# Performance work log

Hardware: AMD Instinct MI355X
Metric: run time of the kernel (lower is better)

Reference implementation:

```python
import jax, jax.numpy as jnp
import numpy as np

MAP_DIM = 2048
HIDDEN_DIM = 768


def setup_inputs() -> dict:
    key = jax.random.key(0)
    k = jax.random.split(key, 8)
    maps = jax.random.normal(k[0], (8, 14, 14, MAP_DIM), dtype=jnp.float32)
    hiddens = jax.random.normal(k[1], (8, 64, HIDDEN_DIM), dtype=jnp.float32)
    s_map = 1.0 / np.sqrt(MAP_DIM)
    s_hid = 1.0 / np.sqrt(HIDDEN_DIM)
    W_map = jax.random.uniform(k[2], (HIDDEN_DIM, MAP_DIM), jnp.float32, -s_map, s_map)
    b_map = jax.random.uniform(k[3], (HIDDEN_DIM,), jnp.float32, -s_map, s_map)
    W_final = jax.random.uniform(k[4], (HIDDEN_DIM, MAP_DIM), jnp.float32, -s_map, s_map)
    b_final = jax.random.uniform(k[5], (HIDDEN_DIM,), jnp.float32, -s_map, s_map)
    W_rect = jax.random.uniform(k[6], (1, HIDDEN_DIM), jnp.float32, -s_hid, s_hid)
    b_rect = jax.random.uniform(k[7], (1,), jnp.float32, -s_hid, s_hid)
    return {"maps": maps, "hiddens": hiddens, "W_map": W_map, "b_map": b_map,
            "W_final": W_final, "b_final": b_final, "W_rect": W_rect, "b_rect": b_rect}


def reference(maps, hiddens, W_map, b_map, W_final, b_final, W_rect, b_rect):
    B = maps.shape[0]
    # flatten spatial dims: (B, P, M)
    fm = maps.reshape(B, -1, maps.shape[-1])
    # map_linear: (B, P, H)
    mlo = jnp.einsum('bpm,hm->bph', fm, W_map) + b_map
    # additive (Bahdanau-style) score tensor: (B, T, P, H)
    rect = jax.nn.relu(mlo[:, None, :, :] + hiddens[:, :, None, :])
    # rectified_linear H -> 1, squeeze: (B, T, P)
    scores = jnp.einsum('btph,h->btp', rect, W_rect[0]) + b_rect[0]
    # softmax over pixels
    attn = jax.nn.softmax(scores, axis=2)  # (B, T, P)
    # weighted sum of flattened maps: (B, T, M)
    ctx = jnp.einsum('btp,bpm->btm', attn, fm)
    out = jnp.einsum('btm,hm->bth', ctx, W_final) + b_final + hiddens
    return out, attn
```

## Files before the change

### kernel.cpp

```cpp
#include <hip/hip_runtime.h>
#include <stdint.h>

#define NB 8
#define NP 196
#define NM 2048
#define NH 768
#define NT 64
#define PPAD 224
#define NROWS (NB*NP)
#define HC 16
#define HCL 48

typedef __attribute__((ext_vector_type(8))) short short8;
typedef __attribute__((ext_vector_type(4))) float floatx4;
typedef __fp16 h2 __attribute__((ext_vector_type(2)));

__device__ __forceinline__ uint16_t f2b_(float f){
    union{float f; uint32_t i;} v; v.f=f; uint32_t x=v.i;
    return (uint16_t)((x + 0x7fffu + ((x>>16)&1u))>>16);
}
__device__ __forceinline__ uint16_t f2h_(float f){
    union{__fp16 h; uint16_t u;} v; v.h = (__fp16)f; return v.u;
}
__device__ __forceinline__ h2 u2h2(uint32_t u){ union{uint32_t u; h2 h;} v; v.u=u; return v.h; }
__device__ __forceinline__ short8 ldsfrag(const uint16_t* p){
    union{ uint4 u; short8 s; } v; v.u = *(const uint4*)p; return v.s;
}

__global__ __launch_bounds__(256)
void cvt3(const float* __restrict__ s0, uint16_t* __restrict__ d0, int n0,
          const float* __restrict__ s1, uint16_t* __restrict__ d1, int n1,
          const float* __restrict__ s2, uint16_t* __restrict__ d2, int n2)
{
    long i = (long)(blockIdx.x*256 + threadIdx.x)*8;
    const float* s; uint16_t* d; long j;
    if (i < n0)                { s=s0; d=d0; j=i; }
    else if (i < (long)n0+n1)  { s=s1; d=d1; j=i-n0; }
    else                       { s=s2; d=d2; j=i-n0-n1; if (j>=n2) return; }
    float4 a = *(const float4*)(s+j);
    float4 b = *(const float4*)(s+j+4);
    uint4 w;
    w.x = (uint32_t)f2b_(a.x) | ((uint32_t)f2b_(a.y)<<16);
    w.y = (uint32_t)f2b_(a.z) | ((uint32_t)f2b_(a.w)<<16);
    w.z = (uint32_t)f2b_(b.x) | ((uint32_t)f2b_(b.y)<<16);
    w.w = (uint32_t)f2b_(b.z) | ((uint32_t)f2b_(b.w)<<16);
    *(uint4*)(d+j) = w;
}

#define LSTR 72
__global__ __launch_bounds__(256)
void k1_tiled(const uint16_t* __restrict__ A, const uint16_t* __restrict__ Bcat,
              const float* __restrict__ bmap, uint16_t* __restrict__ mloT,
              uint16_t* __restrict__ gt)
{
    __shared__ uint16_t sA[64*LSTR];
    __shared__ uint16_t sB[64*LSTR];
    const int tid  = threadIdx.x;
    const int wv   = tid >> 6, lane = tid & 63;
    const int quad = lane >> 4, lq = lane & 15;
    const int m0 = blockIdx.x*64, n0 = blockIdx.y*64;

    const int r0 = tid >> 3, q0 = tid & 7;
    const int r1 = r0 + 32;
    int gar0 = m0 + r0; if (gar0 >= NROWS) gar0 = NROWS-1;
    int gar1 = m0 + r1; if (gar1 >= NROWS) gar1 = NROWS-1;
    const uint16_t* pa0 = A + (size_t)gar0*NM + q0*8;
    const uint16_t* pa1 = A + (size_t)gar1*NM + q0*8;
    const uint16_t* pb0 = Bcat + (size_t)(n0 + r0)*NM + q0*8;
    const uint16_t* pb1 = Bcat + (size_t)(n0 + r1)*NM + q0*8;
    uint16_t* la0 = &sA[r0*LSTR + q0*8];
    uint16_t* la1 = &sA[r1*LSTR + q0*8];
    uint16_t* lb0 = &sB[r0*LSTR + q0*8];
    uint16_t* lb1 = &sB[r1*LSTR + q0*8];

    const int msub = (wv & 1)*32, nsub = (wv >> 1)*32;

    floatx4 acc[2][2];
    #pragma unroll
    for (int i=0;i<2;++i)
        #pragma unroll
        for (int j=0;j<2;++j) acc[i][j] = (floatx4){0.f,0.f,0.f,0.f};

    uint4 va0 = *(const uint4*)pa0, va1 = *(const uint4*)pa1;
    uint4 vb0 = *(const uint4*)pb0, vb1 = *(const uint4*)pb1;

    for (int ks=0; ks<32; ++ks){
        *(uint4*)la0 = va0; *(uint4*)la1 = va1;
        *(uint4*)lb0 = vb0; *(uint4*)lb1 = vb1;
        __syncthreads();
        if (ks < 31){
            const int off = (ks+1)*64;
            va0 = *(const uint4*)(pa0 + off);
            va1 = *(const uint4*)(pa1 + off);
            vb0 = *(const uint4*)(pb0 + off);
            vb1 = *(const uint4*)(pb1 + off);
        }
        #pragma unroll
        for (int kk=0; kk<2; ++kk){
            short8 af[2], bf[2];
            #pragma unroll
            for (int mt=0;mt<2;++mt)
                af[mt] = ldsfrag(&sA[(msub + mt*16 + lq)*LSTR + kk*32 + quad*8]);
            #pragma unroll
            for (int nt=0;nt<2;++nt)
                bf[nt] = ldsfrag(&sB[(nsub + nt*16 + lq)*LSTR + kk*32 + quad*8]);
            #pragma unroll
            for (int mt=0;mt<2;++mt)
                #pragma unroll
                for (int nt=0;nt<2;++nt)
                    acc[mt][nt] = __builtin_amdgcn_mfma_f32_16x16x32_bf16(af[mt], bf[nt], acc[mt][nt], 0,0,0);
        }
        __syncthreads();
    }

    if (n0 < NH){
        #pragma unroll
        for (int nt=0;nt<2;++nt){
            const int col = n0 + nsub + nt*16 + lq;
            const float bv = bmap[col];
            #pragma unroll
            for (int mt=0;mt<2;++mt){
                floatx4 c = acc[mt][nt];
                const int rb = m0 + msub + mt*16 + quad*4;
                #pragma unroll
                for (int r=0;r<4;++r){
                    const int row = rb + r;
                    if (row < NROWS){
                        const int b = row / NP, p = row - b*NP;
                        mloT[((size_t)b*NH + col)*PPAD + p] = f2h_(c[r] + bv);
                    }
                }
            }
        }
    } else {
        #pragma unroll
        for (int nt=0;nt<2;++nt){
            const int h = n0 - NH + nsub + nt*16 + lq;
            #pragma unroll
            for (int mt=0;mt<2;++mt){
                floatx4 c = acc[mt][nt];
                const int rb = m0 + msub + mt*16 + quad*4;
                #pragma unroll
                for (int r=0;r<4;++r){
                    const int row = rb + r;
                    if (row < NROWS){
                        const int b = row / NP, p = row - b*NP;
                        gt[((size_t)b*NH + h)*PPAD + p] = f2b_(c[r]);
                    }
                }
            }
        }
    }
}

__global__ __launch_bounds__(256)
void k2a(const uint16_t* __restrict__ mloT, const float* __restrict__ hid,
         const float* __restrict__ Wrect, float* __restrict__ partial)
{
    const int hcv = blockIdx.x;
    const int tgp = blockIdx.y;
    const int b   = blockIdx.z;
    const int tid = threadIdx.x;
    const int w   = tid >> 6;
    const int L   = tid & 63;
    const int slot = w & 1;
    const int tg   = tgp*2 + (w>>1);
    const int t0   = tg*8;
    const int Lc   = (slot && L > 47) ? 47 : L;
    const int p    = slot*128 + 2*Lc;

    float acc[8][2];
    #pragma unroll
    for (int i=0;i<8;++i){ acc[i][0]=0.f; acc[i][1]=0.f; }

    const uint16_t* mp = mloT + (size_t)b*NH*PPAD + p;
    const float*    hb = hid + ((size_t)b*NT + t0)*NH;
    const int h0 = hcv*HCL;

    #pragma unroll 4
    for (int hh=0; hh<HCL; ++hh){
        const int h = h0 + hh;
        const uint32_t m = *(const uint32_t*)(mp + (size_t)h*PPAD);
        const h2 mh = u2h2(m);
        const float m0f = (float)mh.x;
        const float m1f = (float)mh.y;
        const float wvv = Wrect[h];
        #pragma unroll
        for (int ti=0; ti<8; ++ti){
            const float hv = hb[(size_t)ti*NH + h];
            acc[ti][0] = fmaf(fmaxf(m0f+hv, 0.f), wvv, acc[ti][0]);
            acc[ti][1] = fmaf(fmaxf(m1f+hv, 0.f), wvv, acc[ti][1]);
        }
    }
    #pragma unroll
    for (int ti=0; ti<8; ++ti){
        float2 v = make_float2(acc[ti][0], acc[ti][1]);
        *(float2*)&partial[(((size_t)hcv*NB + b)*NT + t0+ti)*PPAD + p] = v;
    }
}

__global__ __launch_bounds__(256)
void k2b(const float* __restrict__ partial, float* __restrict__ attn_out,
         uint16_t* __restrict__ attnb)
{
    const int bt = blockIdx.x;
    const int tid = threadIdx.x;
    const int lane = tid & 63, wv = tid >> 6;
    __shared__ float s_red[8];

    float s = 0.f;
    if (tid < PPAD){
        #pragma unroll
        for (int hcv=0; hcv<HC; ++hcv)
            s += partial[(((size_t)hcv*NB*NT) + bt)*PPAD + tid];
    }
    float v = (tid < NP) ? s : -3.0e38f;
    #pragma unroll
    for (int off=32; off>0; off>>=1) v = fmaxf(v, __shfl_xor(v, off));
    if (lane == 0) s_red[wv] = v;
    __syncthreads();
    const float mx = fmaxf(fmaxf(s_red[0], s_red[1]), fmaxf(s_red[2], s_red[3]));
    float e = (tid < NP) ? __expf(s - mx) : 0.f;
    float r = e;
    #pragma unroll
    for (int off=32; off>0; off>>=1) r += __shfl_xor(r, off);
    if (lane == 0) s_red[4 + wv] = r;
    __syncthreads();
    const float inv = 1.f / (s_red[4] + s_red[5] + s_red[6] + s_red[7]);
    const float a = e * inv;
    if (tid < NP)   attn_out[(size_t)bt*NP + tid] = a;
    if (tid < PPAD) attnb[(size_t)bt*PPAD + tid] = (tid < NP) ? f2b_(a) : (uint16_t)0;
}

__global__ __launch_bounds__(64)
void k4_small(const uint16_t* __restrict__ attnb, const uint16_t* __restrict__ gt,
              const float* __restrict__ bfin, const float* __restrict__ hid,
              float* __restrict__ out)
{
    const int lane = threadIdx.x;
    const int quad = lane>>4, lq = lane&15;
    const int tt = blockIdx.x;
    const int n0 = blockIdx.y*64;
    const int b  = blockIdx.z;
    const uint16_t* aprow = attnb + ((size_t)b*NT + tt*16 + lq)*PPAD + quad*8;
    const uint16_t* bp[4];
    #pragma unroll
    for (int i=0;i<4;++i) bp[i] = gt + ((size_t)b*NH + n0 + i*16 + lq)*PPAD + quad*8;

    floatx4 acc[4];
    #pragma unroll
    for (int i=0;i<4;++i) acc[i] = (floatx4){0.f,0.f,0.f,0.f};
    #pragma unroll
    for (int ks=0; ks<7; ++ks){
        short8 Af = ldsfrag(aprow + ks*32);
        #pragma unroll
        for (int i=0;i<4;++i)
            acc[i] = __builtin_amdgcn_mfma_f32_16x16x32_bf16(Af, ldsfrag(bp[i] + ks*32), acc[i], 0,0,0);
    }
    #pragma unroll
    for (int ns=0;ns<4;++ns){
        const int col = n0 + ns*16 + lq;
        const float bv = bfin[col];
        floatx4 c = acc[ns];
        #pragma unroll
        for (int r=0;r<4;++r){
            const int row = b*NT + tt*16 + quad*4 + r;
            const size_t idx = (size_t)row*NH + col;
            out[idx] = c[r] + bv + hid[idx];
        }
    }
}

__global__ __launch_bounds__(256)
void k1_map(const float* __restrict__ fm, const float* __restrict__ Wmap,
            const float* __restrict__ bmap, float* __restrict__ mlo)
{
    __shared__ float s_fm[8][NM];
    const int row0 = blockIdx.x*8;
    for (int i=threadIdx.x; i<8*NM; i+=256){
        int r=i>>11, k=i&2047;
        s_fm[r][k] = fm[(size_t)(row0+r)*NM + k];
    }
    __syncthreads();
    #pragma unroll
    for (int it=0; it<3; ++it){
        int c = threadIdx.x + it*256;
        float acc[8];
        #pragma unroll
        for(int r=0;r<8;++r) acc[r]=0.f;
        const float* wr = Wmap + (size_t)c*NM;
        for (int k=0;k<NM;k+=4){
            float4 w4 = *(const float4*)(wr + k);
            #pragma unroll
            for(int r=0;r<8;++r){
                acc[r]=fmaf(w4.x,s_fm[r][k+0],acc[r]);
                acc[r]=fmaf(w4.y,s_fm[r][k+1],acc[r]);
                acc[r]=fmaf(w4.z,s_fm[r][k+2],acc[r]);
                acc[r]=fmaf(w4.w,s_fm[r][k+3],acc[r]);
            }
        }
        float bb = bmap[c];
        for(int r=0;r<8;++r) mlo[(size_t)(row0+r)*NH + c] = acc[r]+bb;
    }
}

__global__ __launch_bounds__(256)
void k2_scores_f(const float* __restrict__ mlo, const float* __restrict__ hid,
                 const float* __restrict__ Wrect, const float* __restrict__ brect,
                 float* __restrict__ attn_out)
{
    const int b    = blockIdx.x >> 4;
    const int tg   = blockIdx.x & 15;
    const int wave = threadIdx.x >> 6;
    const int lane = threadIdx.x & 63;
    const int t    = tg*4 + wave;
    float hv[12], wv[12];
    #pragma unroll
    for (int j=0;j<12;++j){
        int h = lane + 64*j;
        hv[j] = hid[(size_t)(b*NT+t)*NH + h];
        wv[j] = Wrect[h];
    }
    __shared__ float s_sc[4][NP];
    for (int p=0;p<NP;++p){
        const float* mr = mlo + ((size_t)b*NP + p)*NH;
        float acc = 0.f;
        #pragma unroll
        for (int j=0;j<12;++j){
            float v = fmaxf(mr[lane+64*j] + hv[j], 0.f);
            acc = fmaf(v,wv[j],acc);
        }
        #pragma unroll
        for (int off=32; off>0; off>>=1) acc += __shfl_down(acc,off);
        if (lane==0) s_sc[wave][p] = acc;
    }
    __syncthreads();
    float x[4]; int pidx[4];
    #pragma unroll
    for (int i=0;i<4;++i){
        int p = lane + 64*i; pidx[i]=p;
        x[i] = (p<NP) ? s_sc[wave][p] : -3.0e38f;
    }
    float mx = fmaxf(fmaxf(x[0],x[1]),fmaxf(x[2],x[3]));
    #pragma unroll
    for (int off=32; off>0; off>>=1) mx = fmaxf(mx,__shfl_xor(mx,off));
    float sum=0.f;
    #pragma unroll
    for (int i=0;i<4;++i){ x[i] = (pidx[i]<NP) ? __expf(x[i]-mx) : 0.f; sum += x[i]; }
    #pragma unroll
    for (int off=32; off>0; off>>=1) sum += __shfl_xor(sum,off);
    const float inv = 1.f/sum;
    const size_t base = (size_t)(b*NT+t)*NP;
    #pragma unroll
    for (int i=0;i<4;++i) if (pidx[i]<NP) attn_out[base+pidx[i]] = x[i]*inv;
}

__global__ __launch_bounds__(256)
void k3_ctx(const float* __restrict__ attn, const float* __restrict__ fm,
            float* __restrict__ ctx)
{
    const int b  = blockIdx.x >> 4;
    const int tg = blockIdx.x & 15;
    __shared__ float s_a[4][NP];
    for (int i=threadIdx.x; i<4*NP; i+=256){
        int tt=i/NP, p=i-tt*NP;
        s_a[tt][p] = attn[(size_t)(b*NT + tg*4+tt)*NP + p];
    }
    __syncthreads();
    const int m0 = threadIdx.x*8;
    float acc[4][8];
    #pragma unroll
    for(int tt=0;tt<4;++tt)
        #pragma unroll
        for(int i=0;i<8;++i) acc[tt][i]=0.f;
    const float* fb = fm + (size_t)b*NP*NM + m0;
    for (int p=0;p<NP;++p){
        float4 u0 = *(const float4*)(fb + (size_t)p*NM);
        float4 u1 = *(const float4*)(fb + (size_t)p*NM + 4);
        float f[8] = {u0.x,u0.y,u0.z,u0.w,u1.x,u1.y,u1.z,u1.w};
        #pragma unroll
        for(int tt=0;tt<4;++tt){
            float a = s_a[tt][p];
            #pragma unroll
            for(int i=0;i<8;++i) acc[tt][i] = fmaf(a,f[i],acc[tt][i]);
        }
    }
    #pragma unroll
    for(int tt=0;tt<4;++tt){
        float* cr = ctx + (size_t)(b*NT + tg*4+tt)*NM + m0;
        #pragma unroll
        for(int i=0;i<8;++i) cr[i]=acc[tt][i];
    }
}

__global__ __launch_bounds__(256)
void k4_final(const float* __restrict__ ctx, const float* __restrict__ Wfin,
              const float* __restrict__ bfin, const float* __restrict__ hid,
              float* __restrict__ out)
{
    __shared__ float s_c[8][NM];
    const int row0 = blockIdx.x*8;
    for (int i=threadIdx.x; i<8*NM; i+=256){
        int r=i>>11, k=i&2047;
        s_c[r][k] = ctx[(size_t)(row0+r)*NM + k];
    }
    __syncthreads();
    #pragma unroll
    for (int it=0; it<3; ++it){
        int c = threadIdx.x + it*256;
        float acc[8];
        #pragma unroll
        for(int r=0;r<8;++r) acc[r]=0.f;
        const float* wr = Wfin + (size_t)c*NM;
        for (int k=0;k<NM;k+=4){
            float4 w4 = *(const float4*)(wr + k);
            #pragma unroll
            for(int r=0;r<8;++r){
                acc[r]=fmaf(w4.x,s_c[r][k+0],acc[r]);
                acc[r]=fmaf(w4.y,s_c[r][k+1],acc[r]);
                acc[r]=fmaf(w4.z,s_c[r][k+2],acc[r]);
                acc[r]=fmaf(w4.w,s_c[r][k+3],acc[r]);
            }
        }
        float bb = bfin[c];
        for(int r=0;r<8;++r)
            out[(size_t)(row0+r)*NH + c] = acc[r] + bb + hid[(size_t)(row0+r)*NH + c];
    }
}

extern "C" void kernel_launch(void* const* d_in, const int* in_sizes, int n_in,
                              void* d_out, int out_size, void* d_ws, size_t ws_size,
                              hipStream_t stream)
{
    const float* maps  = (const float*)d_in[0];
    const float* hid   = (const float*)d_in[1];
    const float* Wmap  = (const float*)d_in[2];
    const float* bmap  = (const float*)d_in[3];
    const float* Wfin  = (const float*)d_in[4];
    const float* bfin  = (const float*)d_in[5];
    const float* Wrect = (const float*)d_in[6];
    const float* brect = (const float*)d_in[7];

    float* out_ptr  = (float*)d_out;
    float* attn_out = out_ptr + (size_t)NB*NT*NH;

    const int    FME    = NB*NP*NM;
    const int    WE     = NH*NM;
    const size_t fmb_b  = (size_t)FME*2;
    const size_t w_b    = (size_t)WE*2;
    const size_t mloT_b = (size_t)NB*NH*PPAD*2;
    const size_t gt_b   = (size_t)NB*NH*PPAD*2;
    const size_t atb_b  = (size_t)NB*NT*PPAD*2;
    const size_t need   = fmb_b + 2*w_b + mloT_b + gt_b + atb_b;

    if (ws_size >= need) {
        uint16_t* fmb   = (uint16_t*)d_ws;
        uint16_t* wcat  = (uint16_t*)((char*)d_ws + fmb_b);
        uint16_t* wfinb = wcat + (size_t)WE;
        uint16_t* mloT  = (uint16_t*)((char*)d_ws + fmb_b + 2*w_b);
        uint16_t* gt    = mloT + (size_t)NB*NH*PPAD;
        uint16_t* attnb = gt   + (size_t)NB*NH*PPAD;
        float*    partial = (float*)d_ws;

        const int total8 = (FME + 2*WE)/8;
        hipLaunchKernelGGL(cvt3, dim3(total8/256), dim3(256), 0, stream,
                           maps, fmb, FME, Wmap, wcat, WE, Wfin, wfinb, WE);
        hipLaunchKernelGGL(k1_tiled, dim3(25,24), dim3(256), 0, stream,
                           fmb, wcat, bmap, mloT, gt);
        hipLaunchKernelGGL(k2a, dim3(HC,4,NB), dim3(256), 0, stream,
                           mloT, hid, Wrect, partial);
        hipLaunchKernelGGL(k2b, dim3(NB*NT), dim3(256), 0, stream,
                           partial, attn_out, attnb);
        hipLaunchKernelGGL(k4_small, dim3(4,12,NB), dim3(64), 0, stream,
                           attnb, gt, bfin, hid, out_ptr);
    } else {
        float* mlo = (float*)d_ws;
        float* ctx = mlo + (size_t)NB*NP*NH;
        hipLaunchKernelGGL(k1_map,     dim3(NB*NP/8),   dim3(256), 0, stream, maps, Wmap, bmap, mlo);
        hipLaunchKernelGGL(k2_scores_f,dim3(NB*(NT/4)), dim3(256), 0, stream, mlo, hid, Wrect, brect, attn_out);
        hipLaunchKernelGGL(k3_ctx,     dim3(NB*(NT/4)), dim3(256), 0, stream, attn_out, maps, ctx);
        hipLaunchKernelGGL(k4_final,   dim3(NB*NT/8),   dim3(256), 0, stream, ctx, Wfin, bfin, hid, out_ptr);
    }
}
```

Baseline: 136.7 us.

## Use 128x128 GEMM tiles with direct global-to-LDS loads and XOR swizzle

```diff
diff --git a/kernel.cpp b/kernel.cpp
--- a/kernel.cpp
+++ b/kernel.cpp
@@ -25,6 +25,14 @@
 __device__ __forceinline__ h2 u2h2(uint32_t u){ union{uint32_t u; h2 h;} v; v.u=u; return v.h; }
 __device__ __forceinline__ short8 ldsfrag(const uint16_t* p){
     union{ uint4 u; short8 s; } v; v.u = *(const uint4*)p; return v.s;
+}
+__device__ __forceinline__ void gload16(const uint16_t* g, uint16_t* l){
+    __builtin_amdgcn_global_load_lds(
+        reinterpret_cast<const __attribute__((address_space(1))) uint32_t*>(
+            reinterpret_cast<uintptr_t>(g)),
+        reinterpret_cast<__attribute__((address_space(3))) uint32_t*>(
+            reinterpret_cast<uintptr_t>(l)),
+        16, 0, 0);
 }
 
 __global__ __launch_bounds__(256)
@@ -47,106 +55,97 @@
     *(uint4*)(d+j) = w;
 }
 
-#define LSTR 72
-__global__ __launch_bounds__(256)
-void k1_tiled(const uint16_t* __restrict__ A, const uint16_t* __restrict__ Bcat,
-              const float* __restrict__ bmap, uint16_t* __restrict__ mloT,
-              uint16_t* __restrict__ gt)
-{
-    __shared__ uint16_t sA[64*LSTR];
-    __shared__ uint16_t sB[64*LSTR];
-    const int tid  = threadIdx.x;
-    const int wv   = tid >> 6, lane = tid & 63;
-    const int quad = lane >> 4, lq = lane & 15;
-    const int m0 = blockIdx.x*64, n0 = blockIdx.y*64;
-
-    const int r0 = tid >> 3, q0 = tid & 7;
-    const int r1 = r0 + 32;
-    int gar0 = m0 + r0; if (gar0 >= NROWS) gar0 = NROWS-1;
-    int gar1 = m0 + r1; if (gar1 >= NROWS) gar1 = NROWS-1;
-    const uint16_t* pa0 = A + (size_t)gar0*NM + q0*8;
-    const uint16_t* pa1 = A + (size_t)gar1*NM + q0*8;
-    const uint16_t* pb0 = Bcat + (size_t)(n0 + r0)*NM + q0*8;
-    const uint16_t* pb1 = Bcat + (size_t)(n0 + r1)*NM + q0*8;
-    uint16_t* la0 = &sA[r0*LSTR + q0*8];
-    uint16_t* la1 = &sA[r1*LSTR + q0*8];
-    uint16_t* lb0 = &sB[r0*LSTR + q0*8];
-    uint16_t* lb1 = &sB[r1*LSTR + q0*8];
-
-    const int msub = (wv & 1)*32, nsub = (wv >> 1)*32;
-
-    floatx4 acc[2][2];
-    #pragma unroll
-    for (int i=0;i<2;++i)
-        #pragma unroll
-        for (int j=0;j<2;++j) acc[i][j] = (floatx4){0.f,0.f,0.f,0.f};
-
-    uint4 va0 = *(const uint4*)pa0, va1 = *(const uint4*)pa1;
-    uint4 vb0 = *(const uint4*)pb0, vb1 = *(const uint4*)pb1;
+__global__ __launch_bounds__(256)
+void k1_m97(const uint16_t* __restrict__ A, const uint16_t* __restrict__ Bcat,
+            const float* __restrict__ bmap, uint16_t* __restrict__ mloT,
+            uint16_t* __restrict__ gt)
+{
+    __shared__ uint16_t sA[128*64];
+    __shared__ uint16_t sB[128*64];
+    const int tid = threadIdx.x;
+    const int w = tid>>6, lane = tid&63;
+    const int quad = lane>>4, lq = lane&15;
+    const int m0 = blockIdx.x*128, n0 = blockIdx.y*128;
+
+    const int r8 = lane>>3;
+    const int qx = (lane&7) ^ r8;
+    const uint16_t* gsrc[8];
+    uint16_t* ldst[8];
+    #pragma unroll
+    for (int j=0;j<8;++j){
+        const int c = w*8 + j;
+        if (c < 16){
+            gsrc[j] = A + (size_t)(m0 + c*8 + r8)*NM + qx*8;
+            ldst[j] = &sA[c*512];
+        } else {
+            gsrc[j] = Bcat + (size_t)(n0 + (c-16)*8 + r8)*NM + qx*8;
+            ldst[j] = &sB[(c-16)*512];
+        }
+    }
+
+    const int msub = (w&1)*64, nsub = (w>>1)*64;
+    floatx4 acc[16];
+    #pragma unroll
+    for (int i=0;i<16;++i) acc[i] = (floatx4){0.f,0.f,0.f,0.f};
 
     for (int ks=0; ks<32; ++ks){
-        *(uint4*)la0 = va0; *(uint4*)la1 = va1;
-        *(uint4*)lb0 = vb0; *(uint4*)lb1 = vb1;
+        #pragma unroll
+        for (int j=0;j<8;++j) gload16(gsrc[j] + ks*64, ldst[j]);
         __syncthreads();
-        if (ks < 31){
-            const int off = (ks+1)*64;
-            va0 = *(const uint4*)(pa0 + off);
-            va1 = *(const uint4*)(pa1 + off);
-            vb0 = *(const uint4*)(pb0 + off);
-            vb1 = *(const uint4*)(pb1 + off);
-        }
         #pragma unroll
         for (int kk=0; kk<2; ++kk){
-            short8 af[2], bf[2];
-            #pragma unroll
-            for (int mt=0;mt<2;++mt)
-                af[mt] = ldsfrag(&sA[(msub + mt*16 + lq)*LSTR + kk*32 + quad*8]);
-            #pragma unroll
-            for (int nt=0;nt<2;++nt)
-                bf[nt] = ldsfrag(&sB[(nsub + nt*16 + lq)*LSTR + kk*32 + quad*8]);
-            #pragma unroll
-            for (int mt=0;mt<2;++mt)
+            short8 af[4], bf[4];
+            #pragma unroll
+            for (int mt=0;mt<4;++mt){
+                const int r = msub + mt*16 + lq;
+                af[mt] = ldsfrag(&sA[r*64 + (((kk*4+quad) ^ (lq&7))*8)]);
+            }
+            #pragma unroll
+            for (int nt=0;nt<4;++nt){
+                const int r = nsub + nt*16 + lq;
+                bf[nt] = ldsfrag(&sB[r*64 + (((kk*4+quad) ^ (lq&7))*8)]);
+            }
+            #pragma unroll
+            for (int mt=0;mt<4;++mt)
                 #pragma unroll
-                for (int nt=0;nt<2;++nt)
-                    acc[mt][nt] = __builtin_amdgcn_mfma_f32_16x16x32_bf16(af[mt], bf[nt], acc[mt][nt], 0,0,0);
+                for (int nt=0;nt<4;++nt)
+                    acc[mt*4+nt] = __builtin_amdgcn_mfma_f32_16x16x32_bf16(af[mt], bf[nt], acc[mt*4+nt], 0,0,0);
         }
         __syncthreads();
     }
 
     if (n0 < NH){
         #pragma unroll
-        for (int nt=0;nt<2;++nt){
+        for (int nt=0;nt<4;++nt){
             const int col = n0 + nsub + nt*16 + lq;
             const float bv = bmap[col];
             #pragma unroll
-            for (int mt=0;mt<2;++mt){
-                floatx4 c = acc[mt][nt];
-                const int rb = m0 + msub + mt*16 + quad*4;
-                #pragma unroll
-                for (int r=0;r<4;++r){
-                    const int row = rb + r;
-                    if (row < NROWS){
-                        const int b = row / NP, p = row - b*NP;
-                        mloT[((size_t)b*NH + col)*PPAD + p] = f2h_(c[r] + bv);
-                    }
+            for (int mt=0;mt<4;++mt){
+                const int row0r = m0 + msub + mt*16 + quad*4;
+                if (row0r < NROWS){
+                    floatx4 c = acc[mt*4+nt];
+                    const int b = row0r / NP, p0 = row0r - b*NP;
+                    uint2 u;
+                    u.x = (uint32_t)f2h_(c[0]+bv) | ((uint32_t)f2h_(c[1]+bv)<<16);
+                    u.y = (uint32_t)f2h_(c[2]+bv) | ((uint32_t)f2h_(c[3]+bv)<<16);
+                    *(uint2*)&mloT[((size_t)b*NH + col)*PPAD + p0] = u;
                 }
             }
         }
     } else {
         #pragma unroll
-        for (int nt=0;nt<2;++nt){
+        for (int nt=0;nt<4;++nt){
             const int h = n0 - NH + nsub + nt*16 + lq;
             #pragma unroll
-            for (int mt=0;mt<2;++mt){
-                floatx4 c = acc[mt][nt];
-                const int rb = m0 + msub + mt*16 + quad*4;
-                #pragma unroll
-                for (int r=0;r<4;++r){
-                    const int row = rb + r;
-                    if (row < NROWS){
-                        const int b = row / NP, p = row - b*NP;
-                        gt[((size_t)b*NH + h)*PPAD + p] = f2b_(c[r]);
-                    }
+            for (int mt=0;mt<4;++mt){
+                const int row0r = m0 + msub + mt*16 + quad*4;
+                if (row0r < NROWS){
+                    floatx4 c = acc[mt*4+nt];
+                    const int b = row0r / NP, p0 = row0r - b*NP;
+                    uint2 u;
+                    u.x = (uint32_t)f2b_(c[0]) | ((uint32_t)f2b_(c[1])<<16);
+                    u.y = (uint32_t)f2b_(c[2]) | ((uint32_t)f2b_(c[3])<<16);
+                    *(uint2*)&gt[((size_t)b*NH + h)*PPAD + p0] = u;
                 }
             }
         }
@@ -465,7 +464,7 @@
         const int total8 = (FME + 2*WE)/8;
         hipLaunchKernelGGL(cvt3, dim3(total8/256), dim3(256), 0, stream,
                            maps, fmb, FME, Wmap, wcat, WE, Wfin, wfinb, WE);
-        hipLaunchKernelGGL(k1_tiled, dim3(25,24), dim3(256), 0, stream,
+        hipLaunchKernelGGL(k1_m97, dim3(13,12), dim3(256), 0, stream,
                            fmb, wcat, bmap, mloT, gt);
         hipLaunchKernelGGL(k2a, dim3(HC,4,NB), dim3(256), 0, stream,
                            mloT, hid, Wrect, partial);
```

Result: slower. 146.3 us (+7.0%).
